# Performance work log

Hardware: AMD Instinct MI355X
Metric: run time of the kernel (lower is better)

Reference implementation:

```python
import jax, jax.numpy as jnp
import numpy as np

B_REQ = 4      # requests (one LoRA adapter per request, equal-length segments)
SEQ = 1024     # tokens per request (prefill)
HID = 4096
NH = 32        # num_qo_heads == num_kv_heads (MHA)
DH = 128       # head_dim
RANK = 16
ROPE_THETA = 10000.0


def setup_inputs() -> dict:
    key = jax.random.key(0)
    ks = jax.random.split(key, 13)
    T = B_REQ * SEQ
    def w(k, shape, scale):
        return jax.random.normal(k, shape, dtype=jnp.float32) * scale
    inp = {
        "hidden_states": w(ks[0], (T, HID), 1.0),
        # weights stored [in, out] (transpose of nn.Linear.weight); y = x @ W
        "Wq": w(ks[1], (HID, NH * DH), 0.02),
        "Wk": w(ks[2], (HID, NH * DH), 0.02),
        "Wv": w(ks[3], (HID, NH * DH), 0.02),
        "Wo": w(ks[4], (NH * DH, HID), 0.02),
        "Aq": w(ks[5], (B_REQ, HID, RANK), 0.02),
        "Bq": w(ks[6], (B_REQ, RANK, NH * DH), 0.02),
        "Ak": w(ks[7], (B_REQ, HID, RANK), 0.02),
        "Bk": w(ks[8], (B_REQ, RANK, NH * DH), 0.02),
        "Av": w(ks[9], (B_REQ, HID, RANK), 0.02),
        "Bv": w(ks[10], (B_REQ, RANK, NH * DH), 0.02),
        "Ao": w(ks[11], (B_REQ, NH * DH, RANK), 0.02),
        "Bo": w(ks[12], (B_REQ, RANK, HID), 0.02),
    }
    return inp


def _lora(xb, A, B):
    # segment-indexed batched LoRA: per-request adapter. xb: [B,S,Din]
    return jnp.einsum("bsr,bro->bso", jnp.einsum("bsd,bdr->bsr", xb, A), B)


def _rope(x):
    # Llama rotate-half RoPE. x: [B,S,NH,DH]
    half = DH // 2
    inv_freq = 1.0 / (ROPE_THETA ** (jnp.arange(half, dtype=jnp.float32) / half))
    ang = jnp.arange(SEQ, dtype=jnp.float32)[:, None] * inv_freq[None, :]  # [S,half]
    cos = jnp.cos(ang)[None, :, None, :].astype(x.dtype)
    sin = jnp.sin(ang)[None, :, None, :].astype(x.dtype)
    x1, x2 = x[..., :half], x[..., half:]
    return jnp.concatenate([x1 * cos - x2 * sin, x2 * cos + x1 * sin], axis=-1)


def reference(hidden_states, Wq, Wk, Wv, Wo, Aq, Bq, Ak, Bk, Av, Bv, Ao, Bo):
    x = hidden_states.reshape(B_REQ, SEQ, HID)
    # qkv projections + batched multi-tenant LoRA (add_lora)
    q = jnp.einsum("bsd,do->bso", x, Wq) + _lora(x, Aq, Bq)
    k = jnp.einsum("bsd,do->bso", x, Wk) + _lora(x, Ak, Bk)
    v = jnp.einsum("bsd,do->bso", x, Wv) + _lora(x, Av, Bv)
    q = _rope(q.reshape(B_REQ, SEQ, NH, DH))
    k = _rope(k.reshape(B_REQ, SEQ, NH, DH))
    v = v.reshape(B_REQ, SEQ, NH, DH)
    scale = 1.0 / np.sqrt(DH)
    scores = jnp.einsum("bqhd,bkhd->bhqk", q, k) * scale  # [B,NH,S,S]
    causal = jnp.tril(jnp.ones((SEQ, SEQ), dtype=bool))
    scores = jnp.where(causal[None, None], scores, jnp.finfo(scores.dtype).min)
    probs = jax.nn.softmax(scores.astype(jnp.float32), axis=-1).astype(q.dtype)
    attn = jnp.einsum("bhqk,bkhd->bqhd", probs, v).reshape(B_REQ, SEQ, NH * DH)
    # output projection + LoRA on attn output
    o = jnp.einsum("bso,od->bsd", attn, Wo) + _lora(attn, Ao, Bo)
    return o.reshape(B_REQ * SEQ, HID)
```

## Files before the change

kernel.cpp:

```cpp
#include <hip/hip_runtime.h>
#include <cstdint>

#define HID 4096
#define SEQ 1024
#define B_REQ 4
#define NH 32
#define DH 128
#define RANK 16

typedef unsigned short u16;
typedef __attribute__((ext_vector_type(8))) short short8;
typedef __attribute__((ext_vector_type(8))) unsigned short us8;
typedef __attribute__((ext_vector_type(4))) float f32x4;

static __device__ __forceinline__ float bf2f(u16 u) {
  union { unsigned int i; float f; } v; v.i = ((unsigned int)u) << 16; return v.f;
}
static __device__ __forceinline__ u16 f2bf(float f) {
  union { float f; unsigned int i; } v; v.f = f;
  unsigned int r = v.i + 0x7FFFu + ((v.i >> 16) & 1u);
  return (u16)(r >> 16);
}

template<typename T> struct io;
template<> struct io<u16> {
  static __device__ __forceinline__ float ld(const u16* p, size_t i) { return bf2f(p[i]); }
  static __device__ __forceinline__ void st(u16* p, size_t i, float v) { p[i] = f2bf(v); }
};
template<> struct io<float> {
  static __device__ __forceinline__ float ld(const float* p, size_t i) { return p[i]; }
  static __device__ __forceinline__ void st(float* p, size_t i, float v) { p[i] = v; }
};

static __device__ __forceinline__ void ld8f(const u16* p, float* o) {
  us8 v = *(const us8*)p;
#pragma unroll
  for (int i = 0; i < 8; i++) o[i] = bf2f(v[i]);
}
static __device__ __forceinline__ void ld8f(const float* p, float* o) {
  const float4* q = (const float4*)p;
  float4 a = q[0], b = q[1];
  o[0]=a.x; o[1]=a.y; o[2]=a.z; o[3]=a.w; o[4]=b.x; o[5]=b.y; o[6]=b.z; o[7]=b.w;
}

__global__ void detect_k(const u16* __restrict__ w, int* __restrict__ dflag) {
  if (threadIdx.x == 0 && blockIdx.x == 0) {
    int huge = 0;
    for (int i = 0; i < 2048; i++) {
      int e = (w[i] >> 7) & 0xFF;
      if (e >= 0xC0) huge++;
    }
    dflag[0] = (huge > 8) ? 1 : 0;
  }
}

template<typename T>
__global__ __launch_bounds__(256) void convert_k(const int* __restrict__ fl, int want,
    const T* __restrict__ src, u16* __restrict__ dst, int n) {
  if (fl[0] != want) return;
  int stride = gridDim.x * blockDim.x;
  for (int i = blockIdx.x * blockDim.x + threadIdx.x; i < n; i += stride)
    dst[i] = f2bf(io<T>::ld(src, i));
}

template<typename T>
__global__ __launch_bounds__(256) void transpose_k(const int* __restrict__ fl, int want,
    const T* __restrict__ W, u16* __restrict__ Tt) {
  if (fl[0] != want) return;
  __shared__ u16 st[64][68];
  int r0 = blockIdx.y * 64, c0 = blockIdx.x * 64;
  int t = threadIdx.x;
  int r = t >> 2, cb = (t & 3) * 16;
#pragma unroll
  for (int j = 0; j < 16; j++)
    st[r][cb + j] = f2bf(io<T>::ld(W, (size_t)(r0 + r) * HID + c0 + cb + j));
  __syncthreads();
#pragma unroll
  for (int j = 0; j < 4; j++) {
    int cw = cb + j*4;
    ushort4 v;
    v.x = st[cw+0][r]; v.y = st[cw+1][r]; v.z = st[cw+2][r]; v.w = st[cw+3][r];
    *(ushort4*)&Tt[(size_t)(c0 + r) * HID + r0 + cw] = v;
  }
}

template<typename T>
__global__ __launch_bounds__(256) void lora_r_k(const int* __restrict__ fl, int want,
    const u16* __restrict__ X, const T* __restrict__ A0,
    const T* __restrict__ A1, const T* __restrict__ A2, float* __restrict__ R) {
  if (fl[0] != want) return;
  int s = blockIdx.x, b = blockIdx.y, m = blockIdx.z;
  const T* A = (m==0?A0: m==1?A1:A2) + (size_t)b * HID * RANK;
  const u16* x = X + (size_t)(b*SEQ + s) * HID;
  float* r = R + ((size_t)(m*B_REQ + b) * SEQ + s) * RANK;
  int t = threadIdx.x;
  int c = t >> 4;
  float acc = 0.f;
  for (int i = 0; i < 256; i++)
    acc += bf2f(x[c + 16*i]) * io<T>::ld(A, t + 256*i);
  __shared__ float red[256];
  red[t] = acc;
  __syncthreads();
  if (t < 16) {
    float sum = 0.f;
#pragma unroll
    for (int cc = 0; cc < 16; cc++) sum += red[cc*16 + t];
    r[t] = sum;
  }
}

template<typename TOUT>
__global__ __launch_bounds__(256) void gemm_bt_k(const int* __restrict__ fl, int want,
    const u16* __restrict__ A, const u16* __restrict__ BT, TOUT* __restrict__ C) {
  if (want >= 0 && fl[0] != want) return;
  __shared__ u16 sA[128*32];
  __shared__ u16 sB[128*32];
  int tid = threadIdx.x, lane = tid & 63, wave = tid >> 6;
  int l15 = lane & 15, quad = lane >> 4;
  int wm = wave >> 1, wn = wave & 1;
  int m0 = blockIdx.x * 128, n0 = blockIdx.y * 128;
  f32x4 acc[4][4];
  f32x4 zero = {0.f,0.f,0.f,0.f};
#pragma unroll
  for (int i=0;i<4;i++)
#pragma unroll
    for (int j=0;j<4;j++) acc[i][j] = zero;
  const u16* gA = A  + (size_t)(m0 + wave*32 + (lane>>2)) * HID + (lane&3)*8;
  const u16* gB = BT + (size_t)(n0 + wave*32 + (lane>>2)) * HID + (lane&3)*8;
  u16* lA = sA + (wave*32)*32;
  u16* lB = sB + (wave*32)*32;
  for (int k0 = 0; k0 < HID; k0 += 32) {
    __syncthreads();
#pragma unroll
    for (int i = 0; i < 2; i++) {
      __builtin_amdgcn_global_load_lds(
          (const __attribute__((address_space(1))) void*)(gA + (size_t)i*16*HID + k0),
          (__attribute__((address_space(3))) void*)(lA + i*16*32), 16, 0, 0);
      __builtin_amdgcn_global_load_lds(
          (const __attribute__((address_space(1))) void*)(gB + (size_t)i*16*HID + k0),
          (__attribute__((address_space(3))) void*)(lB + i*16*32), 16, 0, 0);
    }
    __syncthreads();
    short8 af[4], bfr[4];
#pragma unroll
    for (int tm=0;tm<4;tm++) af[tm]  = *(const short8*)&sA[(wm*64 + tm*16 + l15)*32 + quad*8];
#pragma unroll
    for (int tn=0;tn<4;tn++) bfr[tn] = *(const short8*)&sB[(wn*64 + tn*16 + l15)*32 + quad*8];
#pragma unroll
    for (int tm=0;tm<4;tm++)
#pragma unroll
      for (int tn=0;tn<4;tn++)
        acc[tm][tn] = __builtin_amdgcn_mfma_f32_16x16x32_bf16(af[tm], bfr[tn], acc[tm][tn], 0, 0, 0);
  }
  int rb = m0 + wm*64 + quad*4;
  int cb = n0 + wn*64 + l15;
#pragma unroll
  for (int tm=0;tm<4;tm++)
#pragma unroll
    for (int tn=0;tn<4;tn++)
#pragma unroll
      for (int rr=0;rr<4;rr++)
        io<TOUT>::st(C, (size_t)(rb + tm*16 + rr) * HID + cb + tn*16, acc[tm][tn][rr]);
}

template<typename T>
__global__ __launch_bounds__(256) void lora_rope_k(const int* __restrict__ fl, int want,
    u16* __restrict__ Qb, u16* __restrict__ Kb, u16* __restrict__ Vb,
    const float* __restrict__ R,
    const T* __restrict__ Bq, const T* __restrict__ Bk, const T* __restrict__ Bv) {
  if (fl[0] != want) return;
  int s0 = blockIdx.x * 4;
  int z = blockIdx.y; int kind = z >> 2, b = z & 3;
  u16* Ob = kind==0?Qb: kind==1?Kb:Vb;
  const T* Bm = (kind==0?Bq: kind==1?Bk:Bv) + (size_t)b * RANK * HID;
  int t = threadIdx.x;
  int h = t >> 3, d0 = (t & 7) * 8;
  int col0 = h*DH + d0, col1 = col0 + 64;
  __shared__ float rr[4][RANK];
  if (t < 64)
    rr[t>>4][t&15] = R[((size_t)(kind*B_REQ + b) * SEQ + s0 + (t>>4)) * RANK + (t&15)];
  __syncthreads();
  float v0[4][8], v1[4][8];
  size_t base = (size_t)(b*SEQ + s0) * HID;
#pragma unroll
  for (int si = 0; si < 4; si++) {
    us8 a = *(const us8*)&Ob[base + (size_t)si*HID + col0];
    us8 c = *(const us8*)&Ob[base + (size_t)si*HID + col1];
#pragma unroll
    for (int i = 0; i < 8; i++) { v0[si][i] = bf2f(a[i]); v1[si][i] = bf2f(c[i]); }
  }
#pragma unroll 4
  for (int j = 0; j < RANK; j++) {
    float b0[8], b1[8];
    ld8f(Bm + (size_t)j*HID + col0, b0);
    ld8f(Bm + (size_t)j*HID + col1, b1);
#pragma unroll
    for (int si = 0; si < 4; si++) {
      float rj = rr[si][j];
#pragma unroll
      for (int i = 0; i < 8; i++) { v0[si][i] += rj*b0[i]; v1[si][i] += rj*b1[i]; }
    }
  }
  if (kind == 2) {
#pragma unroll
    for (int si = 0; si < 4; si++) {
      us8 a, c;
#pragma unroll
      for (int i = 0; i < 8; i++) { a[i] = f2bf(v0[si][i]); c[i] = f2bf(v1[si][i]); }
      *(us8*)&Ob[base + (size_t)si*HID + col0] = a;
      *(us8*)&Ob[base + (size_t)si*HID + col1] = c;
    }
    return;
  }
  float fr[8];
#pragma unroll
  for (int i = 0; i < 8; i++)
    fr[i] = exp2f((float)(d0 + i) * (-13.287712379549449f / 64.f));
#pragma unroll
  for (int si = 0; si < 4; si++) {
    float sa = (float)(s0 + si);
    us8 a, c;
#pragma unroll
    for (int i = 0; i < 8; i++) {
      float sn, cs;
      sincosf(sa * fr[i], &sn, &cs);
      a[i] = f2bf(v0[si][i]*cs - v1[si][i]*sn);
      c[i] = f2bf(v1[si][i]*cs + v0[si][i]*sn);
    }
    *(us8*)&Ob[base + (size_t)si*HID + col0] = a;
    *(us8*)&Ob[base + (size_t)si*HID + col1] = c;
  }
}

__global__ __launch_bounds__(256) void vtrans_k(const u16* __restrict__ V, u16* __restrict__ VT) {
  int st = blockIdx.x, h = blockIdx.y, b = blockIdx.z;
  int s0 = st * 64;
  __shared__ u16 tmp[64][136];
  int t = threadIdx.x;
  int sr = t >> 2, c0 = (t & 3) * 32;
  const u16* vp = V + (size_t)(b*SEQ + s0 + sr) * HID + h*DH + c0;
#pragma unroll
  for (int j = 0; j < 4; j++)
    *(us8*)&tmp[sr][c0 + j*8] = *(const us8*)(vp + j*8);
  __syncthreads();
  int d = t >> 1, so = (t & 1) * 32;
  u16* op = VT + ((size_t)(b*NH + h) * DH + d) * SEQ + s0 + so;
#pragma unroll
  for (int j = 0; j < 4; j++) {
    us8 v;
#pragma unroll
    for (int i = 0; i < 8; i++) ((u16*)&v)[i] = tmp[so + j*8 + i][d];
    *(us8*)(op + j*8) = v;
  }
}

__global__ __launch_bounds__(256) void attn_k(
    const u16* __restrict__ Q, const u16* __restrict__ K, const u16* __restrict__ VT,
    u16* __restrict__ O) {
  int qb = (int)gridDim.x - 1 - (int)blockIdx.x;
  int h = blockIdx.y, b = blockIdx.z;
  int q0 = qb * 64;
  int tid = threadIdx.x, lane = tid & 63, wave = tid >> 6;
  int l15 = lane & 15, quad = lane >> 4;
  __shared__ u16 sK[64*136];
  __shared__ u16 sVT[128*72];
  __shared__ u16 sP[4][16*72];
  short8 qf[4];
  {
    const u16* qp = Q + (size_t)(b*SEQ + q0 + wave*16 + l15) * HID + h*DH + quad*8;
#pragma unroll
    for (int c = 0; c < 4; c++) qf[c] = *(const short8*)(qp + c*32);
  }
  f32x4 zero = {0.f,0.f,0.f,0.f};
  f32x4 oacc[8];
#pragma unroll
  for (int i=0;i<8;i++) oacc[i] = zero;
  float m_i[4], l_i[4];
#pragma unroll
  for (int r=0;r<4;r++){ m_i[r] = -1e30f; l_i[r] = 0.f; }
  int krow = tid >> 2, kcol = (tid & 3) * 32;
  int vrow = tid >> 1, vcol = (tid & 1) * 32;
  const u16* kbase = K + (size_t)(b*SEQ) * HID + h*DH;
  const u16* vbase = VT + (size_t)(b*NH + h) * DH * SEQ;
  int nkt = qb + 1;
  for (int kt = 0; kt < nkt; kt++) {
    int k0 = kt * 64;
    __syncthreads();
    {
      const u16* kp = kbase + (size_t)(k0 + krow) * HID + kcol;
#pragma unroll
      for (int j = 0; j < 4; j++)
        *(us8*)&sK[krow*136 + kcol + j*8] = *(const us8*)(kp + j*8);
      const u16* vp = vbase + (size_t)vrow * SEQ + k0 + vcol;
#pragma unroll
      for (int j = 0; j < 4; j++)
        *(us8*)&sVT[vrow*72 + vcol + j*8] = *(const us8*)(vp + j*8);
    }
    __syncthreads();
    int q_hi = q0 + wave*16 + 15;
    if (k0 <= q_hi) {
      f32x4 sc4[4];
#pragma unroll
      for (int g=0;g<4;g++) sc4[g] = zero;
#pragma unroll
      for (int c = 0; c < 4; c++) {
#pragma unroll
        for (int g = 0; g < 4; g++) {
          short8 kf = *(const short8*)&sK[(g*16 + l15)*136 + c*32 + quad*8];
          sc4[g] = __builtin_amdgcn_mfma_f32_16x16x32_bf16(qf[c], kf, sc4[g], 0,0,0);
        }
      }
      const float scale = 0.08838834764831845f;
      float alpha[4], pst[4][4];
#pragma unroll
      for (int r = 0; r < 4; r++) {
        int q_abs = q0 + wave*16 + quad*4 + r;
        float v[4];
#pragma unroll
        for (int g = 0; g < 4; g++) {
          v[g] = sc4[g][r] * scale;
          if (k0 + g*16 + l15 > q_abs) v[g] = -1e30f;
        }
        float mx = fmaxf(fmaxf(v[0],v[1]), fmaxf(v[2],v[3]));
#pragma unroll
        for (int sh = 1; sh < 16; sh <<= 1) mx = fmaxf(mx, __shfl_xor(mx, sh, 64));
        float mnew = fmaxf(m_i[r], mx);
        float a = __expf(m_i[r] - mnew);
        float rs = 0.f;
#pragma unroll
        for (int g = 0; g < 4; g++) { float p = __expf(v[g] - mnew); pst[g][r] = p; rs += p; }
#pragma unroll
        for (int sh = 1; sh < 16; sh <<= 1) rs += __shfl_xor(rs, sh, 64);
        l_i[r] = a * l_i[r] + rs;
        m_i[r] = mnew;
        alpha[r] = a;
      }
#pragma unroll
      for (int dt=0; dt<8; dt++)
#pragma unroll
        for (int r=0;r<4;r++) oacc[dt][r] *= alpha[r];
#pragma unroll
      for (int g = 0; g < 4; g++)
#pragma unroll
        for (int r = 0; r < 4; r++)
          sP[wave][(quad*4+r)*72 + g*16 + l15] = f2bf(pst[g][r]);
      asm volatile("s_waitcnt lgkmcnt(0)" ::: "memory");
      short8 pf0 = *(const short8*)&sP[wave][l15*72 + quad*8];
      short8 pf1 = *(const short8*)&sP[wave][l15*72 + 32 + quad*8];
#pragma unroll
      for (int dt = 0; dt < 8; dt++) {
        short8 vf0 = *(const short8*)&sVT[(dt*16 + l15)*72 + quad*8];
        short8 vf1 = *(const short8*)&sVT[(dt*16 + l15)*72 + 32 + quad*8];
        oacc[dt] = __builtin_amdgcn_mfma_f32_16x16x32_bf16(pf0, vf0, oacc[dt], 0,0,0);
        oacc[dt] = __builtin_amdgcn_mfma_f32_16x16x32_bf16(pf1, vf1, oacc[dt], 0,0,0);
      }
    }
  }
  u16* op = O + (size_t)(b*SEQ + q0 + wave*16 + quad*4) * HID + h*DH + l15;
#pragma unroll
  for (int dt=0; dt<8; dt++)
#pragma unroll
    for (int r=0;r<4;r++) {
      float v = oacc[dt][r] / l_i[r];
      op[(size_t)r * HID + dt*16] = f2bf(v);
    }
}

template<typename T>
__global__ __launch_bounds__(256) void out_add_k(const int* __restrict__ fl, int want,
    const float* __restrict__ Ro, const T* __restrict__ Bo, T* __restrict__ Out) {
  if (fl[0] != want) return;
  int c = blockIdx.x * 256 + threadIdx.x;
  int s = blockIdx.y, b = blockIdx.z;
  __shared__ float rr[RANK];
  if (threadIdx.x < RANK) rr[threadIdx.x] = Ro[((size_t)(b*SEQ + s)) * RANK + threadIdx.x];
  __syncthreads();
  size_t row = (size_t)(b*SEQ + s);
  float val = io<T>::ld(Out, row*HID + c);
  const T* bo = Bo + (size_t)b * RANK * HID;
#pragma unroll
  for (int j = 0; j < RANK; j++) val += rr[j] * io<T>::ld(bo, (size_t)j*HID + c);
  io<T>::st(Out, row*HID + c, val);
}

extern "C" void kernel_launch(void* const* d_in, const int* in_sizes, int n_in,
                              void* d_out, int out_size, void* d_ws, size_t ws_size,
                              hipStream_t stream) {
  char* ws = (char*)d_ws;
  const size_t MAT = (size_t)4096 * 4096 * 2;
  u16* slot0 = (u16*)(ws + 0*MAT);
  u16* slot1 = (u16*)(ws + 1*MAT);
  u16* slot2 = (u16*)(ws + 2*MAT);
  u16* X_bf  = (u16*)(ws + 3*MAT);
  float* r_all = (float*)(ws + 4*MAT);
  float* r_o   = (float*)(ws + 4*MAT + (size_t)3*B_REQ*SEQ*RANK*sizeof(float));
  int* dflag   = (int*)(ws + 4*MAT + (size_t)4*B_REQ*SEQ*RANK*sizeof(float));

  u16* q_lin = (u16*)d_out;
  u16* k_lin = slot1;
  u16* v_lin = slot2;
  u16* attnb = slot0;

  const int NX = B_REQ * SEQ * HID;

  detect_k<<<1, 64, 0, stream>>>((const u16*)d_in[1], dflag);

#define BOTH(call_b, call_f) do { call_b; call_f; } while (0)
  BOTH((convert_k<u16>  <<<8192,256,0,stream>>>(dflag,0,(const u16*)  d_in[0], X_bf, NX)),
       (convert_k<float><<<8192,256,0,stream>>>(dflag,1,(const float*)d_in[0], X_bf, NX)));
  BOTH((lora_r_k<u16>  <<<dim3(SEQ,B_REQ,3),256,0,stream>>>(dflag,0,X_bf,(const u16*)d_in[5],(const u16*)d_in[7],(const u16*)d_in[9],r_all)),
       (lora_r_k<float><<<dim3(SEQ,B_REQ,3),256,0,stream>>>(dflag,1,X_bf,(const float*)d_in[5],(const float*)d_in[7],(const float*)d_in[9],r_all)));

  u16* lin[3] = { q_lin, k_lin, v_lin };
  for (int m = 0; m < 3; m++) {
    BOTH((transpose_k<u16>  <<<dim3(64,64),256,0,stream>>>(dflag,0,(const u16*)  d_in[1+m], slot0)),
         (transpose_k<float><<<dim3(64,64),256,0,stream>>>(dflag,1,(const float*)d_in[1+m], slot0)));
    gemm_bt_k<u16><<<dim3(32,32),256,0,stream>>>(dflag,-1, X_bf, slot0, lin[m]);
  }
  BOTH((lora_rope_k<u16>  <<<dim3(SEQ/4,12),256,0,stream>>>(dflag,0,q_lin,k_lin,v_lin,r_all,(const u16*)d_in[6],(const u16*)d_in[8],(const u16*)d_in[10])),
       (lora_rope_k<float><<<dim3(SEQ/4,12),256,0,stream>>>(dflag,1,q_lin,k_lin,v_lin,r_all,(const float*)d_in[6],(const float*)d_in[8],(const float*)d_in[10])));

  vtrans_k<<<dim3(SEQ/64,NH,B_REQ),256,0,stream>>>(v_lin, X_bf);

  attn_k<<<dim3(16,NH,B_REQ),256,0,stream>>>(q_lin, k_lin, X_bf, attnb);

  BOTH((lora_r_k<u16>  <<<dim3(SEQ,B_REQ,1),256,0,stream>>>(dflag,0,attnb,(const u16*)d_in[11],(const u16*)d_in[11],(const u16*)d_in[11],r_o)),
       (lora_r_k<float><<<dim3(SEQ,B_REQ,1),256,0,stream>>>(dflag,1,attnb,(const float*)d_in[11],(const float*)d_in[11],(const float*)d_in[11],r_o)));
  BOTH((transpose_k<u16>  <<<dim3(64,64),256,0,stream>>>(dflag,0,(const u16*)  d_in[4], slot1)),
       (transpose_k<float><<<dim3(64,64),256,0,stream>>>(dflag,1,(const float*)d_in[4], slot1)));
  BOTH((gemm_bt_k<u16>  <<<dim3(32,32),256,0,stream>>>(dflag,0, attnb, slot1, (u16*)d_out)),
       (gemm_bt_k<float><<<dim3(32,32),256,0,stream>>>(dflag,1, attnb, slot1, (float*)d_out)));
  BOTH((out_add_k<u16>  <<<dim3(16,SEQ,B_REQ),256,0,stream>>>(dflag,0,r_o,(const u16*)d_in[12],(u16*)d_out)),
       (out_add_k<float><<<dim3(16,SEQ,B_REQ),256,0,stream>>>(dflag,1,r_o,(const float*)d_in[12],(float*)d_out)));
#undef BOTH
}
```

Baseline: 1.732 ms.

## Replace GEMM with 256x256 double-buffered swizzled-LDS pipelined MFMA kernel

New measurement: 1.506 ms. 1.15x faster.

```diff
diff --git a/kernel.cpp b/kernel.cpp
--- a/kernel.cpp
+++ b/kernel.cpp
@@ -109,58 +109,127 @@
   }
 }
 
+#define GMFMA __builtin_amdgcn_mfma_f32_16x16x32_bf16
+#define WAITV4 asm volatile("s_waitcnt vmcnt(4)" ::: "memory")
+#define WAITV0 asm volatile("s_waitcnt vmcnt(0)" ::: "memory")
+#define WAITL0 asm volatile("s_waitcnt lgkmcnt(0)" ::: "memory")
+#define SBAR   __builtin_amdgcn_s_barrier()
+#define SCHED0 __builtin_amdgcn_sched_barrier(0)
+
+#define LDA(BUF,QM,MF,KH) \
+  (*(const short8*)((const char*)(&lds[BUF][0][0]) + \
+     (((QM)*128 + wm*64 + (MF)*16 + l15) * 128) + (((KH)*64 + quad*16) ^ ((l15 & 7) << 4))))
+#define LDB(BUF,QN,NF,KH) \
+  (*(const short8*)((const char*)(&lds[BUF][1][0]) + \
+     (((QN)*128 + wn*32 + (NF)*16 + l15) * 128) + (((KH)*64 + quad*16) ^ ((l15 & 7) << 4))))
+
+#define MFMA_BLK(QM,QN,A0,A1,A2,A3,B0,B1) \
+    acc[(QM)*4+0][(QN)*2+0] = GMFMA(A0,B0,acc[(QM)*4+0][(QN)*2+0],0,0,0); \
+    acc[(QM)*4+1][(QN)*2+0] = GMFMA(A1,B0,acc[(QM)*4+1][(QN)*2+0],0,0,0); \
+    acc[(QM)*4+2][(QN)*2+0] = GMFMA(A2,B0,acc[(QM)*4+2][(QN)*2+0],0,0,0); \
+    acc[(QM)*4+3][(QN)*2+0] = GMFMA(A3,B0,acc[(QM)*4+3][(QN)*2+0],0,0,0); \
+    acc[(QM)*4+0][(QN)*2+1] = GMFMA(A0,B1,acc[(QM)*4+0][(QN)*2+1],0,0,0); \
+    acc[(QM)*4+1][(QN)*2+1] = GMFMA(A1,B1,acc[(QM)*4+1][(QN)*2+1],0,0,0); \
+    acc[(QM)*4+2][(QN)*2+1] = GMFMA(A2,B1,acc[(QM)*4+2][(QN)*2+1],0,0,0); \
+    acc[(QM)*4+3][(QN)*2+1] = GMFMA(A3,B1,acc[(QM)*4+3][(QN)*2+1],0,0,0);
+
+#define PHASE(BUF, QM, QN, STAGE) do { \
+    short8 a00=LDA(BUF,QM,0,0), a10=LDA(BUF,QM,1,0), a20=LDA(BUF,QM,2,0), a30=LDA(BUF,QM,3,0); \
+    short8 a01=LDA(BUF,QM,0,1), a11=LDA(BUF,QM,1,1), a21=LDA(BUF,QM,2,1), a31=LDA(BUF,QM,3,1); \
+    short8 b00=LDB(BUF,QN,0,0), b10=LDB(BUF,QN,1,0); \
+    short8 b01=LDB(BUF,QN,0,1), b11=LDB(BUF,QN,1,1); \
+    STAGE; \
+    WAITV4; SCHED0; \
+    SBAR; \
+    WAITL0; SCHED0; \
+    __builtin_amdgcn_s_setprio(1); \
+    MFMA_BLK(QM,QN,a00,a10,a20,a30,b00,b10) \
+    MFMA_BLK(QM,QN,a01,a11,a21,a31,b01,b11) \
+    __builtin_amdgcn_s_setprio(0); \
+    SBAR; \
+  } while (0)
+
+#define PHASE_TAIL(BUF, QM, QN) do { \
+    short8 a00=LDA(BUF,QM,0,0), a10=LDA(BUF,QM,1,0), a20=LDA(BUF,QM,2,0), a30=LDA(BUF,QM,3,0); \
+    short8 a01=LDA(BUF,QM,0,1), a11=LDA(BUF,QM,1,1), a21=LDA(BUF,QM,2,1), a31=LDA(BUF,QM,3,1); \
+    short8 b00=LDB(BUF,QN,0,0), b10=LDB(BUF,QN,1,0); \
+    short8 b01=LDB(BUF,QN,0,1), b11=LDB(BUF,QN,1,1); \
+    WAITL0; SCHED0; \
+    __builtin_amdgcn_s_setprio(1); \
+    MFMA_BLK(QM,QN,a00,a10,a20,a30,b00,b10) \
+    MFMA_BLK(QM,QN,a01,a11,a21,a31,b01,b11) \
+    __builtin_amdgcn_s_setprio(0); \
+  } while (0)
+
 template<typename TOUT>
-__global__ __launch_bounds__(256) void gemm_bt_k(const int* __restrict__ fl, int want,
+__global__ __launch_bounds__(512, 2) void gemm256_k(const int* __restrict__ fl, int want,
     const u16* __restrict__ A, const u16* __restrict__ BT, TOUT* __restrict__ C) {
   if (want >= 0 && fl[0] != want) return;
-  __shared__ u16 sA[128*32];
-  __shared__ u16 sB[128*32];
-  int tid = threadIdx.x, lane = tid & 63, wave = tid >> 6;
-  int l15 = lane & 15, quad = lane >> 4;
-  int wm = wave >> 1, wn = wave & 1;
-  int m0 = blockIdx.x * 128, n0 = blockIdx.y * 128;
-  f32x4 acc[4][4];
+  __shared__ u16 lds[2][2][256*64];
+  const int tid = threadIdx.x, lane = tid & 63, wave = tid >> 6;
+  const int l15 = lane & 15, quad = lane >> 4;
+  const int wm = wave >> 2, wn = wave & 3;
+  int bid = blockIdx.x;
+  int swz = (bid & 7) * 32 + (bid >> 3);
+  const int m0 = (swz >> 4) * 256, n0 = (swz & 15) * 256;
+  const int r = tid >> 3;
+  const int ce = ((((tid & 7) * 16) ^ ((r & 7) << 4)) >> 1);
+
+  auto stA = [&](int nb, int ht, int kt) {
+    const u16* s0 = A + (size_t)(m0 + ht*64 + r)       * HID + kt*64 + ce;
+    const u16* s1 = A + (size_t)(m0 + 128 + ht*64 + r) * HID + kt*64 + ce;
+    u16* d0 = &lds[nb][0][(ht*128 + wave*8) * 64];
+    u16* d1 = &lds[nb][0][(ht*128 + 64 + wave*8) * 64];
+    __builtin_amdgcn_global_load_lds((const __attribute__((address_space(1))) void*)s0,
+        (__attribute__((address_space(3))) void*)d0, 16, 0, 0);
+    __builtin_amdgcn_global_load_lds((const __attribute__((address_space(1))) void*)s1,
+        (__attribute__((address_space(3))) void*)d1, 16, 0, 0);
+  };
+  auto stB = [&](int nb, int qn, int kt) {
+    const u16* s0 = BT + (size_t)(n0 + (r>>5)*64 + qn*32 + (r&31))       * HID + kt*64 + ce;
+    const u16* s1 = BT + (size_t)(n0 + 128 + (r>>5)*64 + qn*32 + (r&31)) * HID + kt*64 + ce;
+    u16* d0 = &lds[nb][1][(qn*128 + wave*8) * 64];
+    u16* d1 = &lds[nb][1][(qn*128 + 64 + wave*8) * 64];
+    __builtin_amdgcn_global_load_lds((const __attribute__((address_space(1))) void*)s0,
+        (__attribute__((address_space(3))) void*)d0, 16, 0, 0);
+    __builtin_amdgcn_global_load_lds((const __attribute__((address_space(1))) void*)s1,
+        (__attribute__((address_space(3))) void*)d1, 16, 0, 0);
+  };
+
+  f32x4 acc[8][4];
   f32x4 zero = {0.f,0.f,0.f,0.f};
 #pragma unroll
-  for (int i=0;i<4;i++)
+  for (int i=0;i<8;i++)
 #pragma unroll
     for (int j=0;j<4;j++) acc[i][j] = zero;
-  const u16* gA = A  + (size_t)(m0 + wave*32 + (lane>>2)) * HID + (lane&3)*8;
-  const u16* gB = BT + (size_t)(n0 + wave*32 + (lane>>2)) * HID + (lane&3)*8;
-  u16* lA = sA + (wave*32)*32;
-  u16* lB = sB + (wave*32)*32;
-  for (int k0 = 0; k0 < HID; k0 += 32) {
-    __syncthreads();
-#pragma unroll
-    for (int i = 0; i < 2; i++) {
-      __builtin_amdgcn_global_load_lds(
-          (const __attribute__((address_space(1))) void*)(gA + (size_t)i*16*HID + k0),
-          (__attribute__((address_space(3))) void*)(lA + i*16*32), 16, 0, 0);
-      __builtin_amdgcn_global_load_lds(
-          (const __attribute__((address_space(1))) void*)(gB + (size_t)i*16*HID + k0),
-          (__attribute__((address_space(3))) void*)(lB + i*16*32), 16, 0, 0);
-    }
-    __syncthreads();
-    short8 af[4], bfr[4];
-#pragma unroll
-    for (int tm=0;tm<4;tm++) af[tm]  = *(const short8*)&sA[(wm*64 + tm*16 + l15)*32 + quad*8];
-#pragma unroll
-    for (int tn=0;tn<4;tn++) bfr[tn] = *(const short8*)&sB[(wn*64 + tn*16 + l15)*32 + quad*8];
-#pragma unroll
-    for (int tm=0;tm<4;tm++)
-#pragma unroll
-      for (int tn=0;tn<4;tn++)
-        acc[tm][tn] = __builtin_amdgcn_mfma_f32_16x16x32_bf16(af[tm], bfr[tn], acc[tm][tn], 0, 0, 0);
-  }
-  int rb = m0 + wm*64 + quad*4;
-  int cb = n0 + wn*64 + l15;
-#pragma unroll
-  for (int tm=0;tm<4;tm++)
-#pragma unroll
-    for (int tn=0;tn<4;tn++)
-#pragma unroll
-      for (int rr=0;rr<4;rr++)
-        io<TOUT>::st(C, (size_t)(rb + tm*16 + rr) * HID + cb + tn*16, acc[tm][tn][rr]);
+
+  stA(0,0,0); stB(0,0,0); stA(0,1,0); stB(0,1,0);
+  WAITV4; SCHED0;
+  SBAR;
+
+  for (int tt = 0; tt < 31; ++tt) {
+    int kn = tt*2 + 1;
+    PHASE(0,0,0, stA(1,0,kn)); PHASE(0,1,0, stB(1,0,kn));
+    PHASE(0,0,1, stA(1,1,kn)); PHASE(0,1,1, stB(1,1,kn));
+    PHASE(1,0,0, stA(0,0,kn+1)); PHASE(1,1,0, stB(0,0,kn+1));
+    PHASE(1,0,1, stA(0,1,kn+1)); PHASE(1,1,1, stB(0,1,kn+1));
+  }
+  PHASE(0,0,0, stA(1,0,63)); PHASE(0,1,0, stB(1,0,63));
+  PHASE(0,0,1, stA(1,1,63)); PHASE(0,1,1, stB(1,1,63));
+  WAITV0; SCHED0;
+  SBAR;
+  PHASE_TAIL(1,0,0); PHASE_TAIL(1,1,0); PHASE_TAIL(1,0,1); PHASE_TAIL(1,1,1);
+
+  const int crow = m0 + wm*128 + quad*4;
+  const int ccol = n0 + wn*64 + l15;
+#pragma unroll
+  for (int mfi = 0; mfi < 8; mfi++)
+#pragma unroll
+    for (int nfi = 0; nfi < 4; nfi++)
+#pragma unroll
+      for (int rr = 0; rr < 4; rr++)
+        io<TOUT>::st(C, (size_t)(crow + (mfi>>2)*64 + (mfi&3)*16 + rr) * HID
+                        + ccol + (nfi>>1)*32 + (nfi&1)*16, acc[mfi][nfi][rr]);
 }
 
 template<typename T>
@@ -415,7 +484,7 @@
   for (int m = 0; m < 3; m++) {
     BOTH((transpose_k<u16>  <<<dim3(64,64),256,0,stream>>>(dflag,0,(const u16*)  d_in[1+m], slot0)),
          (transpose_k<float><<<dim3(64,64),256,0,stream>>>(dflag,1,(const float*)d_in[1+m], slot0)));
-    gemm_bt_k<u16><<<dim3(32,32),256,0,stream>>>(dflag,-1, X_bf, slot0, lin[m]);
+    gemm256_k<u16><<<256,512,0,stream>>>(dflag,-1, X_bf, slot0, lin[m]);
   }
   BOTH((lora_rope_k<u16>  <<<dim3(SEQ/4,12),256,0,stream>>>(dflag,0,q_lin,k_lin,v_lin,r_all,(const u16*)d_in[6],(const u16*)d_in[8],(const u16*)d_in[10])),
        (lora_rope_k<float><<<dim3(SEQ/4,12),256,0,stream>>>(dflag,1,q_lin,k_lin,v_lin,r_all,(const float*)d_in[6],(const float*)d_in[8],(const float*)d_in[10])));
@@ -428,8 +497,8 @@
        (lora_r_k<float><<<dim3(SEQ,B_REQ,1),256,0,stream>>>(dflag,1,attnb,(const float*)d_in[11],(const float*)d_in[11],(const float*)d_in[11],r_o)));
   BOTH((transpose_k<u16>  <<<dim3(64,64),256,0,stream>>>(dflag,0,(const u16*)  d_in[4], slot1)),
        (transpose_k<float><<<dim3(64,64),256,0,stream>>>(dflag,1,(const float*)d_in[4], slot1)));
-  BOTH((gemm_bt_k<u16>  <<<dim3(32,32),256,0,stream>>>(dflag,0, attnb, slot1, (u16*)d_out)),
-       (gemm_bt_k<float><<<dim3(32,32),256,0,stream>>>(dflag,1, attnb, slot1, (float*)d_out)));
+  BOTH((gemm256_k<u16>  <<<256,512,0,stream>>>(dflag,0, attnb, slot1, (u16*)d_out)),
+       (gemm256_k<float><<<256,512,0,stream>>>(dflag,1, attnb, slot1, (float*)d_out)));
   BOTH((out_add_k<u16>  <<<dim3(16,SEQ,B_REQ),256,0,stream>>>(dflag,0,r_o,(const u16*)d_in[12],(u16*)d_out)),
        (out_add_k<float><<<dim3(16,SEQ,B_REQ),256,0,stream>>>(dflag,1,r_o,(const float*)d_in[12],(float*)d_out)));
 #undef BOTH
```
